# Optimization experiments

Hardware: AMD Instinct MI355X
Metric: run time of the kernel (lower is better)

Reference implementation:

```python
import jax, jax.numpy as jnp
import numpy as np

B, S = 8, 1024          # sequences, uniform seqlen (cu_seqlens = arange(B+1)*S)
H, HID = 16, 2048       # num_heads, hidden_size
D = HID // H            # head_size = 128


def setup_inputs() -> dict:
    key = jax.random.key(0)
    k0, k1, k2 = jax.random.split(key, 3)
    T = B * S
    hidden_states = jax.random.normal(k0, (T, HID), jnp.float32)
    # FastLinear after prepare_weights stores weight transposed: [in, out]
    w_attn = jax.random.normal(k1, (HID, HID + 2 * D), jnp.float32) * 0.02
    b_attn = jnp.zeros((HID + 2 * D,), jnp.float32)
    w_proj = jax.random.normal(k2, (HID, HID), jnp.float32) * 0.02
    b_proj = jnp.zeros((HID,), jnp.float32)
    cu_seqlens = jnp.arange(B + 1, dtype=jnp.int32) * S
    layer_past = jnp.zeros((T, 2, 1, D), jnp.float32)
    return {
        "hidden_states": hidden_states,
        "w_attn": w_attn,
        "b_attn": b_attn,
        "w_proj": w_proj,
        "b_proj": b_proj,
        "cu_seqlens": cu_seqlens,
        "max_s": S,
        "layer_past": layer_past,
    }


def reference(hidden_states, w_attn, b_attn, w_proj, b_proj, cu_seqlens, max_s, layer_past):
    # Prefill branch: causal MQA flash attention; layer_past is written (cache)
    # but the returned output does not depend on it.
    scale = D ** -0.5
    qkv = hidden_states @ w_attn + b_attn                 # [T, HID + 2D]
    q = qkv[:, :HID].reshape(B, S, H, D)                  # [B,S,H,D]
    kv = qkv[:, HID:].reshape(B, S, 2, D)
    k = kv[:, :, 0]                                       # [B,S,D] single KV head
    v = kv[:, :, 1]                                       # [B,S,D]
    scores = jnp.einsum('bqhd,bkd->bhqk', q, k) * scale   # [B,H,S,S]
    causal = jnp.tril(jnp.ones((S, S), dtype=bool))
    scores = jnp.where(causal, scores, jnp.finfo(scores.dtype).min)
    probs = jax.nn.softmax(scores, axis=-1)
    attn = jnp.einsum('bhqk,bkd->bqhd', probs, v)         # [B,S,H,D]
    attn = attn.reshape(B * S, HID)
    return attn @ w_proj + b_proj                         # [T, HID]
```

## Files before the change

### kernel.cpp

```cpp
#include <hip/hip_runtime.h>
#include <hip/hip_bf16.h>

typedef __hip_bfloat16 bf16;
typedef __attribute__((ext_vector_type(8))) __bf16 bf16x8;
typedef __attribute__((ext_vector_type(4))) float f32x4;
typedef __attribute__((ext_vector_type(16))) float f32x16;
typedef __attribute__((ext_vector_type(8))) short s16x8;
typedef __attribute__((ext_vector_type(4))) unsigned u32x4;

#define B_    8
#define S_    1024
#define H_    16
#define D_    128
#define HID_  2048
#define NQKV_ 2304
#define T_    8192

__device__ __forceinline__ void gload_lds16(const void* g, void* l) {
  __builtin_amdgcn_global_load_lds((const __attribute__((address_space(1))) void*)g,
                                   (__attribute__((address_space(3))) void*)l, 16, 0, 0);
}

__device__ __forceinline__ unsigned pack_bf16(float lo, float hi) {
  return ((unsigned)__bfloat16_as_ushort(__float2bfloat16(hi)) << 16) |
         (unsigned)__bfloat16_as_ushort(__float2bfloat16(lo));
}

__global__ void cast_bf16_kernel(const float* __restrict__ src, bf16* __restrict__ dst, int n8) {
  const int i = blockIdx.x * 256 + threadIdx.x;
  if (i >= n8) return;
  const float4 a = ((const float4*)src)[2 * i];
  const float4 b = ((const float4*)src)[2 * i + 1];
  s16x8 o;
  o[0] = (short)__bfloat16_as_ushort(__float2bfloat16(a.x));
  o[1] = (short)__bfloat16_as_ushort(__float2bfloat16(a.y));
  o[2] = (short)__bfloat16_as_ushort(__float2bfloat16(a.z));
  o[3] = (short)__bfloat16_as_ushort(__float2bfloat16(a.w));
  o[4] = (short)__bfloat16_as_ushort(__float2bfloat16(b.x));
  o[5] = (short)__bfloat16_as_ushort(__float2bfloat16(b.y));
  o[6] = (short)__bfloat16_as_ushort(__float2bfloat16(b.z));
  o[7] = (short)__bfloat16_as_ushort(__float2bfloat16(b.w));
  ((s16x8*)dst)[i] = o;
}

__global__ void transpose_cast_kernel(const float* __restrict__ src, bf16* __restrict__ dst,
                                      int R, int C) {
  __shared__ float tile[32][33];
  const int tx = threadIdx.x & 31, ty = threadIdx.x >> 5;
  const int rt = blockIdx.y * 32, ct = blockIdx.x * 32;
#pragma unroll
  for (int k = 0; k < 4; ++k)
    tile[ty + 8 * k][tx] = src[(size_t)(rt + ty + 8 * k) * C + ct + tx];
  __syncthreads();
#pragma unroll
  for (int k = 0; k < 4; ++k)
    dst[(size_t)(ct + ty + 8 * k) * R + rt + tx] = __float2bfloat16(tile[tx][ty + 8 * k]);
}

__global__ void transpose_v_kernel(const bf16* __restrict__ QKV, bf16* __restrict__ Vt) {
  __shared__ short t[64][72];
  const int kt = blockIdx.x, dt = blockIdx.y, b = blockIdx.z;
  const int r = threadIdx.x >> 3;
  const int c8 = (threadIdx.x & 7) * 8;
#pragma unroll
  for (int p = 0; p < 2; ++p) {
    const int row = p * 32 + r;
    const s16x8 v = *(const s16x8*)(QKV + (size_t)(b * S_ + kt * 64 + row) * NQKV_ +
                                    HID_ + D_ + dt * 64 + c8);
    *(s16x8*)&t[row][c8] = v;
  }
  __syncthreads();
#pragma unroll
  for (int p = 0; p < 2; ++p) {
    const int drow = p * 32 + r;
    s16x8 o;
#pragma unroll
    for (int j = 0; j < 8; ++j) o[j] = t[c8 + j][drow];
    *(s16x8*)(Vt + (size_t)(b * D_ + dt * 64 + drow) * S_ + kt * 64 + c8) = o;
  }
}

template <bool OUT_F32>
__global__ __launch_bounds__(256, 2) void gemm_kernel(const bf16* __restrict__ A,
                                                      const bf16* __restrict__ Bt,
                                                      const float* __restrict__ bias,
                                                      void* __restrict__ Cout,
                                                      int M, int N, int K) {
  __shared__ char lds[65536];
  const int tid = threadIdx.x;
  const int lane = tid & 63;
  const int wave = tid >> 6;

  const int gx = gridDim.x;
  const int lid = blockIdx.y * gx + blockIdx.x;
  const int cpx = (gx * gridDim.y) >> 3;
  const int swz = (lid & 7) * cpx + (lid >> 3);
  const int bn = swz % gx, bm = swz / gx;

  const int lrow = lane & 15, lk = lane >> 4;
  const int rbase = (wave >> 1) * 64;
  const int nbase = (wave & 1) * 64;
  f32x4 acc[4][4] = {};

  int srow[4], scol[4];
#pragma unroll
  for (int o = 0; o < 4; ++o) {
    const int X = o * 4096 + tid * 16;
    const int r = X >> 7, Y = X & 127;
    srow[o] = r;
    scol[o] = Y ^ ((r & 7) << 4);
  }

  const char* Ab = (const char*)A + (size_t)(bm * 128) * K * 2;
  const char* Bb = (const char*)Bt + (size_t)(bn * 128) * K * 2;

#define G_STAGE(buf, kt_)                                                              \
  _Pragma("unroll") for (int o = 0; o < 4; ++o)                                        \
      gload_lds16(Ab + (size_t)srow[o] * (K * 2) + (size_t)(kt_) * 128 + scol[o],      \
                  lds + (buf) + o * 4096 + tid * 16);                                  \
  _Pragma("unroll") for (int o = 0; o < 4; ++o)                                        \
      gload_lds16(Bb + (size_t)srow[o] * (K * 2) + (size_t)(kt_) * 128 + scol[o],      \
                  lds + (buf) + 16384 + o * 4096 + tid * 16);

  G_STAGE(0, 0);

  const int nkt = K >> 6;
  for (int kt = 0; kt < nkt; ++kt) {
    const int cur = (kt & 1) * 32768;
    if (kt < nkt - 1) {
      G_STAGE(cur ^ 32768, kt + 1);
      asm volatile("s_waitcnt vmcnt(8)" ::: "memory");
    } else {
      asm volatile("s_waitcnt vmcnt(0)" ::: "memory");
    }
    __builtin_amdgcn_s_barrier();

    bf16x8 af[4][2], bfr[4][2];
#pragma unroll
    for (int mi = 0; mi < 4; ++mi) {
      const int row = rbase + mi * 16 + lrow;
#pragma unroll
      for (int kk = 0; kk < 2; ++kk)
        af[mi][kk] =
            *(const bf16x8*)(lds + cur + row * 128 + ((kk * 64 + lk * 16) ^ ((row & 7) << 4)));
    }
#pragma unroll
    for (int ni = 0; ni < 4; ++ni) {
      const int row = nbase + ni * 16 + lrow;
#pragma unroll
      for (int kk = 0; kk < 2; ++kk)
        bfr[ni][kk] = *(const bf16x8*)(lds + cur + 16384 + row * 128 +
                                       ((kk * 64 + lk * 16) ^ ((row & 7) << 4)));
    }
#pragma unroll
    for (int kk = 0; kk < 2; ++kk)
#pragma unroll
      for (int mi = 0; mi < 4; ++mi)
#pragma unroll
        for (int ni = 0; ni < 4; ++ni)
          acc[mi][ni] =
              __builtin_amdgcn_mfma_f32_16x16x32_bf16(af[mi][kk], bfr[ni][kk], acc[mi][ni], 0, 0, 0);
    __builtin_amdgcn_s_barrier();
  }
#undef G_STAGE

#pragma unroll
  for (int ni = 0; ni < 4; ++ni) {
    const int col = bn * 128 + nbase + ni * 16 + lrow;
    const float bv = bias[col];
#pragma unroll
    for (int mi = 0; mi < 4; ++mi) {
      const int row0 = bm * 128 + rbase + mi * 16 + lk * 4;
#pragma unroll
      for (int r = 0; r < 4; ++r) {
        const float v = acc[mi][ni][r] + bv;
        if (OUT_F32)
          ((float*)Cout)[(size_t)(row0 + r) * N + col] = v;
        else
          ((bf16*)Cout)[(size_t)(row0 + r) * N + col] = __float2bfloat16(v);
      }
    }
  }
}

__global__ __launch_bounds__(512, 2) void attn_kernel(const bf16* __restrict__ QKV,
                                                      const bf16* __restrict__ Vt,
                                                      bf16* __restrict__ aout) {
  const int pairid = blockIdx.x;
  const int h = blockIdx.y;
  const int b = blockIdx.z;
  const int tid = threadIdx.x;
  const int l = tid & 63;
  const int w = tid >> 6;
  const int ql = l & 31;
  const int hi = l >> 5;

  __shared__ char lds[49152];

  const char* qkv_b = (const char*)QKV + (size_t)b * S_ * (NQKV_ * 2);
  const char* vt_b = (const char*)Vt + (size_t)b * D_ * S_ * 2;

  int kr[2], kc[2], vr[2], vc[2];
#pragma unroll
  for (int o = 0; o < 2; ++o) {
    const int X = o * 8192 + tid * 16;
    const int r = X >> 8;
    kr[o] = r;
    kc[o] = (X & 255) ^ ((r & 15) << 4);
    const int d = X >> 7;
    vr[o] = d;
    vc[o] = (X & 127) ^ ((d & 7) << 4);
  }

#define STAGE_K(kb_off, kt_)                                                          \
  _Pragma("unroll") for (int o = 0; o < 2; ++o)                                       \
      gload_lds16(qkv_b + (size_t)((kt_) * 64 + kr[o]) * (NQKV_ * 2) + HID_ * 2 +     \
                      kc[o],                                                          \
                  lds + (kb_off) + o * 8192 + tid * 16);
#define STAGE_V(kt_)                                                                  \
  _Pragma("unroll") for (int o = 0; o < 2; ++o)                                       \
      gload_lds16(vt_b + (size_t)vr[o] * (S_ * 2) + (kt_) * 128 + vc[o],              \
                  lds + 32768 + o * 8192 + tid * 16);

  for (int pass = 0; pass < 2; ++pass) {
    const int qt = pass == 0 ? (3 - pairid) : pairid;

    bf16x8 qf[8];
#pragma unroll
    for (int p = 0; p < 2; ++p) {
#pragma unroll
      for (int o = 0; o < 4; ++o) {
        const int X = o * 8192 + tid * 16;
        const int r = X >> 8;
        const int cb = (X & 255) ^ ((r & 15) << 4);
        gload_lds16(qkv_b + (size_t)(qt * 256 + p * 128 + r) * (NQKV_ * 2) + h * 256 + cb,
                    lds + X);
      }
      asm volatile("s_waitcnt vmcnt(0)" ::: "memory");
      __builtin_amdgcn_s_barrier();
      if ((w >> 2) == p) {
        const int qrow = (w & 3) * 32 + ql;
#pragma unroll
        for (int ds = 0; ds < 8; ++ds)
          qf[ds] = *(const bf16x8*)(lds + qrow * 256 + ((ds * 32 + hi * 16) ^ ((qrow & 15) << 4)));
      }
      asm volatile("s_waitcnt lgkmcnt(0)" ::: "memory");
      __builtin_amdgcn_sched_barrier(0);
      __builtin_amdgcn_s_barrier();
    }

    STAGE_K(0, 0);

    const float scale = 0.08838834764831845f;
    const int qglob = qt * 256 + w * 32 + ql;
    float mrun = -1e30f, lrun = 0.f;
    f32x16 Oacc[4] = {};

    const int nkt = 4 * qt + 4;
    for (int kt = 0; kt < nkt; ++kt) {
      const int kb = (kt & 1) * 16384;
      STAGE_V(kt);
      if (kt < nkt - 1) {
        STAGE_K(kb ^ 16384, kt + 1);
        asm volatile("s_waitcnt vmcnt(4)" ::: "memory");
      } else {
        asm volatile("s_waitcnt vmcnt(2)" ::: "memory");
      }
      __builtin_amdgcn_s_barrier();
      __builtin_amdgcn_sched_barrier(0);

      const bool skip = (64 * kt >= 256 * qt + 32 * w + 32);
      bf16x8 pa[4];
      if (!skip) {
        const bool need_mask = (64 * kt + 63 > 256 * qt + 32 * w);

        f32x16 s0 = {}, s1 = {};
        __builtin_amdgcn_s_setprio(1);
#pragma unroll
        for (int ds = 0; ds < 8; ++ds) {
          const int krow = ql;
          const bf16x8 kf =
              *(const bf16x8*)(lds + kb + krow * 256 + ((ds * 32 + hi * 16) ^ ((krow & 15) << 4)));
          s0 = __builtin_amdgcn_mfma_f32_32x32x16_bf16(kf, qf[ds], s0, 0, 0, 0);
        }
#pragma unroll
        for (int ds = 0; ds < 8; ++ds) {
          const int krow = 32 + ql;
          const bf16x8 kf =
              *(const bf16x8*)(lds + kb + krow * 256 + ((ds * 32 + hi * 16) ^ ((krow & 15) << 4)));
          s1 = __builtin_amdgcn_mfma_f32_32x32x16_bf16(kf, qf[ds], s1, 0, 0, 0);
        }
        __builtin_amdgcn_s_setprio(0);

#pragma unroll
        for (int r = 0; r < 16; ++r) {
          const int krl = (r & 3) + 8 * (r >> 2) + 4 * hi;
          float v0 = s0[r] * scale, v1 = s1[r] * scale;
          if (need_mask) {
            if (64 * kt + krl > qglob) v0 = -1e30f;
            if (64 * kt + 32 + krl > qglob) v1 = -1e30f;
          }
          s0[r] = v0;
          s1[r] = v1;
        }

        float a0 = -1e30f, a1 = -1e30f, a2 = -1e30f, a3 = -1e30f;
#pragma unroll
        for (int r = 0; r < 16; r += 4) {
          a0 = fmaxf(a0, fmaxf(s0[r], s1[r]));
          a1 = fmaxf(a1, fmaxf(s0[r + 1], s1[r + 1]));
          a2 = fmaxf(a2, fmaxf(s0[r + 2], s1[r + 2]));
          a3 = fmaxf(a3, fmaxf(s0[r + 3], s1[r + 3]));
        }
        float tmax = fmaxf(fmaxf(a0, a1), fmaxf(a2, a3));
        tmax = fmaxf(tmax, __shfl_xor(tmax, 32));

        if (!__all(tmax <= mrun + 8.f)) {
          const float mn = fmaxf(mrun, tmax);
          const float corr = __expf(mrun - mn);
          mrun = mn;
          lrun *= corr;
#pragma unroll
          for (int r = 0; r < 16; ++r) {
            const float cq = __shfl(corr, (r & 3) + 8 * (r >> 2) + 4 * hi);
#pragma unroll
            for (int dt = 0; dt < 4; ++dt) Oacc[dt][r] *= cq;
          }
        }

        float b0 = 0.f, b1 = 0.f, b2 = 0.f, b3 = 0.f;
#pragma unroll
        for (int r = 0; r < 16; r += 4) {
          s0[r] = __expf(s0[r] - mrun);
          s1[r] = __expf(s1[r] - mrun);
          b0 += s0[r] + s1[r];
          s0[r + 1] = __expf(s0[r + 1] - mrun);
          s1[r + 1] = __expf(s1[r + 1] - mrun);
          b1 += s0[r + 1] + s1[r + 1];
          s0[r + 2] = __expf(s0[r + 2] - mrun);
          s1[r + 2] = __expf(s1[r + 2] - mrun);
          b2 += s0[r + 2] + s1[r + 2];
          s0[r + 3] = __expf(s0[r + 3] - mrun);
          s1[r + 3] = __expf(s1[r + 3] - mrun);
          b3 += s0[r + 3] + s1[r + 3];
        }
        float rs = (b0 + b1) + (b2 + b3);
        rs += __shfl_xor(rs, 32);
        lrun += rs;

        unsigned c[16], xc[16];
#pragma unroll
        for (int m = 0; m < 8; ++m) {
          c[m] = pack_bf16(s0[2 * m], s0[2 * m + 1]);
          c[8 + m] = pack_bf16(s1[2 * m], s1[2 * m + 1]);
        }
#pragma unroll
        for (int m = 0; m < 16; ++m) xc[m] = (unsigned)__shfl_xor((int)c[m], 32);

#pragma unroll
        for (int kh = 0; kh < 2; ++kh) {
          const int base = 8 * kh;
          u32x4 f0, f1;
          f0[0] = hi ? xc[base + 2] : c[base + 0];
          f0[1] = hi ? xc[base + 3] : c[base + 1];
          f0[2] = hi ? c[base + 2] : xc[base + 0];
          f0[3] = hi ? c[base + 3] : xc[base + 1];
          f1[0] = hi ? xc[base + 6] : c[base + 4];
          f1[1] = hi ? xc[base + 7] : c[base + 5];
          f1[2] = hi ? c[base + 6] : xc[base + 4];
          f1[3] = hi ? c[base + 7] : xc[base + 5];
          pa[2 * kh] = __builtin_bit_cast(bf16x8, f0);
          pa[2 * kh + 1] = __builtin_bit_cast(bf16x8, f1);
        }
      }

      if (kt < nkt - 1)
        asm volatile("s_waitcnt vmcnt(2)" ::: "memory");
      else
        asm volatile("s_waitcnt vmcnt(0)" ::: "memory");
      __builtin_amdgcn_s_barrier();
      __builtin_amdgcn_sched_barrier(0);

      if (!skip) {
        __builtin_amdgcn_s_setprio(1);
#pragma unroll
        for (int dt = 0; dt < 4; ++dt) {
          const int vrow = dt * 32 + ql;
#pragma unroll
          for (int ks = 0; ks < 4; ++ks) {
            const bf16x8 vf = *(const bf16x8*)(lds + 32768 + vrow * 128 +
                                               ((ks * 32 + hi * 16) ^ ((vrow & 7) << 4)));
            Oacc[dt] = __builtin_amdgcn_mfma_f32_32x32x16_bf16(pa[ks], vf, Oacc[dt], 0, 0, 0);
          }
        }
        __builtin_amdgcn_s_setprio(0);
      }
      __builtin_amdgcn_s_barrier();
    }

#pragma unroll
    for (int r = 0; r < 16; ++r) {
      const int qi = (r & 3) + 8 * (r >> 2) + 4 * hi;
      const float lr = __shfl(lrun, qi);
      const float inv = 1.0f / lr;
      const int token = b * S_ + qt * 256 + w * 32 + qi;
      bf16* orow = aout + (size_t)token * HID_ + h * D_;
#pragma unroll
      for (int dt = 0; dt < 4; ++dt)
        orow[dt * 32 + ql] = __float2bfloat16(Oacc[dt][r] * inv);
    }
    __builtin_amdgcn_s_barrier();
  }
#undef STAGE_K
#undef STAGE_V
}

extern "C" void kernel_launch(void* const* d_in, const int* in_sizes, int n_in,
                              void* d_out, int out_size, void* d_ws, size_t ws_size,
                              hipStream_t stream) {
  const float* hidden = (const float*)d_in[0];
  const float* w_attn = (const float*)d_in[1];
  const float* b_attn = (const float*)d_in[2];
  const float* w_proj = (const float*)d_in[3];
  const float* b_proj = (const float*)d_in[4];

  char* ws = (char*)d_ws;
  char* dob = (char*)d_out;

  bf16* Xbf = (bf16*)ws;
  bf16* WpT = (bf16*)(ws + 33554432);
  bf16* QKV = (bf16*)dob;
  bf16* WaT = (bf16*)(dob + 37748736);
  bf16* Vt = (bf16*)(dob + 50331648);

  cast_bf16_kernel<<<(T_ * HID_) / 8 / 256, 256, 0, stream>>>(hidden, Xbf, (T_ * HID_) / 8);
  transpose_cast_kernel<<<dim3(NQKV_ / 32, HID_ / 32), 256, 0, stream>>>(w_attn, WaT, HID_, NQKV_);
  transpose_cast_kernel<<<dim3(HID_ / 32, HID_ / 32), 256, 0, stream>>>(w_proj, WpT, HID_, HID_);

  gemm_kernel<false><<<dim3(NQKV_ / 128, T_ / 128), 256, 0, stream>>>(
      Xbf, WaT, b_attn, QKV, T_, NQKV_, HID_);

  transpose_v_kernel<<<dim3(S_ / 64, D_ / 64, B_), 256, 0, stream>>>(QKV, Vt);

  attn_kernel<<<dim3(2, H_, B_), 512, 0, stream>>>(QKV, Vt, Xbf);

  gemm_kernel<true><<<dim3(HID_ / 128, T_ / 128), 256, 0, stream>>>(
      Xbf, WpT, b_proj, (float*)d_out, T_, HID_, HID_);
}
```

Measured before the change: 263.1 us.

## Enlarge GEMM tiles to 256x256 with 8 waves and phased load/MFMA interleave

The bf16 GEMM kernel moves from 128x128 tiles with 4 waves to 256x256 tiles with 8 waves and 128KB of double-buffered LDS. Each K-step is split into four sub-tile MFMA phases, with prefetch of the next stage issued in halves between them and MFMA priority raised via setprio. The aim is more data reuse per byte loaded and better overlap of global loads with MFMA work. The cost is fewer workgroups (for example 9x32 for the QKV GEMM), likely occupancy of one block per CU given the LDS size, and more barriers per K-step.

```diff
diff --git a/kernel.cpp b/kernel.cpp
--- a/kernel.cpp
+++ b/kernel.cpp
@@ -81,15 +81,18 @@
 }
 
 template <bool OUT_F32>
-__global__ __launch_bounds__(256, 2) void gemm_kernel(const bf16* __restrict__ A,
+__global__ __launch_bounds__(512, 2) void gemm_kernel(const bf16* __restrict__ A,
                                                       const bf16* __restrict__ Bt,
                                                       const float* __restrict__ bias,
                                                       void* __restrict__ Cout,
                                                       int M, int N, int K) {
-  __shared__ char lds[65536];
+  __shared__ char lds[131072];
   const int tid = threadIdx.x;
   const int lane = tid & 63;
   const int wave = tid >> 6;
+  const int wm = wave >> 2;
+  const int wn = wave & 3;
+  const int lrow = lane & 15, lk = lane >> 4;
 
   const int gx = gridDim.x;
   const int lid = blockIdx.y * gx + blockIdx.x;
@@ -97,90 +100,114 @@
   const int swz = (lid & 7) * cpx + (lid >> 3);
   const int bn = swz % gx, bm = swz / gx;
 
-  const int lrow = lane & 15, lk = lane >> 4;
-  const int rbase = (wave >> 1) * 64;
-  const int nbase = (wave & 1) * 64;
-  f32x4 acc[4][4] = {};
-
-  int srow[4], scol[4];
-#pragma unroll
-  for (int o = 0; o < 4; ++o) {
-    const int X = o * 4096 + tid * 16;
-    const int r = X >> 7, Y = X & 127;
+  f32x4 acc[2][2][4][2] = {};
+
+  int srow[2], scol[2];
+#pragma unroll
+  for (int o = 0; o < 2; ++o) {
+    const int X = o * 8192 + tid * 16;
+    const int r = X >> 7;
     srow[o] = r;
-    scol[o] = Y ^ ((r & 7) << 4);
-  }
-
-  const char* Ab = (const char*)A + (size_t)(bm * 128) * K * 2;
-  const char* Bb = (const char*)Bt + (size_t)(bn * 128) * K * 2;
-
-#define G_STAGE(buf, kt_)                                                              \
-  _Pragma("unroll") for (int o = 0; o < 4; ++o)                                        \
-      gload_lds16(Ab + (size_t)srow[o] * (K * 2) + (size_t)(kt_) * 128 + scol[o],      \
-                  lds + (buf) + o * 4096 + tid * 16);                                  \
-  _Pragma("unroll") for (int o = 0; o < 4; ++o)                                        \
-      gload_lds16(Bb + (size_t)srow[o] * (K * 2) + (size_t)(kt_) * 128 + scol[o],      \
-                  lds + (buf) + 16384 + o * 4096 + tid * 16);
-
-  G_STAGE(0, 0);
-
+    scol[o] = (X & 127) ^ ((r & 7) << 4);
+  }
+
+  const char* Ab = (const char*)A + (size_t)(bm * 256) * K * 2;
+  const char* Bb = (const char*)Bt + (size_t)(bn * 256) * K * 2;
+
+#define STG_HALF(src_base, matoff, half, cbuf, kt_)                                     \
+  _Pragma("unroll") for (int o = 0; o < 2; ++o)                                         \
+      gload_lds16((src_base) + (size_t)((half) * 128 + srow[o]) * (K * 2) +             \
+                      (size_t)(kt_) * 128 + scol[o],                                    \
+                  lds + (cbuf) + (matoff) + (half) * 16384 + o * 8192 + tid * 16);
+
+#define RD_A(cbuf, msub)                                                                \
+  _Pragma("unroll") for (int mi = 0; mi < 4; ++mi)                                      \
+  _Pragma("unroll") for (int kk = 0; kk < 2; ++kk) {                                    \
+    const int row = (msub) * 128 + wm * 64 + mi * 16 + lrow;                            \
+    af[msub][mi][kk] = *(const bf16x8*)(lds + (cbuf) + row * 128 +                      \
+                                        ((kk * 64 + lk * 16) ^ ((row & 7) << 4)));      \
+  }
+#define RD_B(cbuf, nsub)                                                                \
+  _Pragma("unroll") for (int ni = 0; ni < 2; ++ni)                                      \
+  _Pragma("unroll") for (int kk = 0; kk < 2; ++kk) {                                    \
+    const int row = (nsub) * 128 + wn * 32 + ni * 16 + lrow;                            \
+    bf[nsub][ni][kk] = *(const bf16x8*)(lds + (cbuf) + 32768 + row * 128 +              \
+                                        ((kk * 64 + lk * 16) ^ ((row & 7) << 4)));      \
+  }
+#define PH_MFMA(MS, NS)                                                                 \
+  asm volatile("s_waitcnt lgkmcnt(0)" ::: "memory");                                    \
+  __builtin_amdgcn_sched_barrier(0);                                                    \
+  __builtin_amdgcn_s_setprio(1);                                                        \
+  _Pragma("unroll") for (int kk = 0; kk < 2; ++kk)                                      \
+  _Pragma("unroll") for (int mi = 0; mi < 4; ++mi)                                      \
+  _Pragma("unroll") for (int ni = 0; ni < 2; ++ni)                                      \
+    acc[MS][NS][mi][ni] = __builtin_amdgcn_mfma_f32_16x16x32_bf16(                      \
+        af[MS][mi][kk], bf[NS][ni][kk], acc[MS][NS][mi][ni], 0, 0, 0);                  \
+  __builtin_amdgcn_s_setprio(0);
+
+  STG_HALF(Ab, 0, 0, 0, 0);
+  STG_HALF(Ab, 0, 1, 0, 0);
+  STG_HALF(Bb, 32768, 0, 0, 0);
+  STG_HALF(Bb, 32768, 1, 0, 0);
+
+  bf16x8 af[2][4][2], bf[2][2][2];
   const int nkt = K >> 6;
   for (int kt = 0; kt < nkt; ++kt) {
-    const int cur = (kt & 1) * 32768;
-    if (kt < nkt - 1) {
-      G_STAGE(cur ^ 32768, kt + 1);
-      asm volatile("s_waitcnt vmcnt(8)" ::: "memory");
-    } else {
+    const int cb = (kt & 1) * 65536;
+    const int nb = cb ^ 65536;
+    const bool pre = (kt + 1 < nkt);
+    asm volatile("s_waitcnt vmcnt(2)" ::: "memory");
+    __builtin_amdgcn_s_barrier();
+    RD_A(cb, 0);
+    RD_B(cb, 0);
+    if (pre) STG_HALF(Ab, 0, 0, nb, kt + 1);
+    __builtin_amdgcn_s_barrier();
+    PH_MFMA(0, 0);
+    __builtin_amdgcn_s_barrier();
+    RD_A(cb, 1);
+    if (pre) STG_HALF(Ab, 0, 1, nb, kt + 1);
+    __builtin_amdgcn_s_barrier();
+    PH_MFMA(1, 0);
+    if (pre)
+      asm volatile("s_waitcnt vmcnt(4)" ::: "memory");
+    else
       asm volatile("s_waitcnt vmcnt(0)" ::: "memory");
-    }
-    __builtin_amdgcn_s_barrier();
-
-    bf16x8 af[4][2], bfr[4][2];
-#pragma unroll
-    for (int mi = 0; mi < 4; ++mi) {
-      const int row = rbase + mi * 16 + lrow;
-#pragma unroll
-      for (int kk = 0; kk < 2; ++kk)
-        af[mi][kk] =
-            *(const bf16x8*)(lds + cur + row * 128 + ((kk * 64 + lk * 16) ^ ((row & 7) << 4)));
-    }
-#pragma unroll
-    for (int ni = 0; ni < 4; ++ni) {
-      const int row = nbase + ni * 16 + lrow;
-#pragma unroll
-      for (int kk = 0; kk < 2; ++kk)
-        bfr[ni][kk] = *(const bf16x8*)(lds + cur + 16384 + row * 128 +
-                                       ((kk * 64 + lk * 16) ^ ((row & 7) << 4)));
-    }
-#pragma unroll
-    for (int kk = 0; kk < 2; ++kk)
-#pragma unroll
-      for (int mi = 0; mi < 4; ++mi)
-#pragma unroll
-        for (int ni = 0; ni < 4; ++ni)
-          acc[mi][ni] =
-              __builtin_amdgcn_mfma_f32_16x16x32_bf16(af[mi][kk], bfr[ni][kk], acc[mi][ni], 0, 0, 0);
-    __builtin_amdgcn_s_barrier();
-  }
-#undef G_STAGE
-
-#pragma unroll
-  for (int ni = 0; ni < 4; ++ni) {
-    const int col = bn * 128 + nbase + ni * 16 + lrow;
-    const float bv = bias[col];
-#pragma unroll
-    for (int mi = 0; mi < 4; ++mi) {
-      const int row0 = bm * 128 + rbase + mi * 16 + lk * 4;
-#pragma unroll
-      for (int r = 0; r < 4; ++r) {
-        const float v = acc[mi][ni][r] + bv;
-        if (OUT_F32)
-          ((float*)Cout)[(size_t)(row0 + r) * N + col] = v;
-        else
-          ((bf16*)Cout)[(size_t)(row0 + r) * N + col] = __float2bfloat16(v);
-      }
-    }
-  }
+    __builtin_amdgcn_s_barrier();
+    RD_B(cb, 1);
+    if (pre) STG_HALF(Bb, 32768, 0, nb, kt + 1);
+    __builtin_amdgcn_s_barrier();
+    PH_MFMA(0, 1);
+    __builtin_amdgcn_s_barrier();
+    if (pre) STG_HALF(Bb, 32768, 1, nb, kt + 1);
+    PH_MFMA(1, 1);
+    __builtin_amdgcn_s_barrier();
+  }
+#undef STG_HALF
+#undef RD_A
+#undef RD_B
+#undef PH_MFMA
+
+#pragma unroll
+  for (int ms = 0; ms < 2; ++ms)
+#pragma unroll
+    for (int ns = 0; ns < 2; ++ns)
+#pragma unroll
+      for (int ni = 0; ni < 2; ++ni) {
+        const int col = bn * 256 + ns * 128 + wn * 32 + ni * 16 + lrow;
+        const float bv = bias[col];
+#pragma unroll
+        for (int mi = 0; mi < 4; ++mi) {
+          const int row0 = bm * 256 + ms * 128 + wm * 64 + mi * 16 + lk * 4;
+#pragma unroll
+          for (int r = 0; r < 4; ++r) {
+            const float v = acc[ms][ns][mi][ni][r] + bv;
+            if (OUT_F32)
+              ((float*)Cout)[(size_t)(row0 + r) * N + col] = v;
+            else
+              ((bf16*)Cout)[(size_t)(row0 + r) * N + col] = __float2bfloat16(v);
+          }
+        }
+      }
 }
 
 __global__ __launch_bounds__(512, 2) void attn_kernel(const bf16* __restrict__ QKV,
@@ -437,13 +464,13 @@
   transpose_cast_kernel<<<dim3(NQKV_ / 32, HID_ / 32), 256, 0, stream>>>(w_attn, WaT, HID_, NQKV_);
   transpose_cast_kernel<<<dim3(HID_ / 32, HID_ / 32), 256, 0, stream>>>(w_proj, WpT, HID_, HID_);
 
-  gemm_kernel<false><<<dim3(NQKV_ / 128, T_ / 128), 256, 0, stream>>>(
+  gemm_kernel<false><<<dim3(NQKV_ / 256, T_ / 256), 512, 0, stream>>>(
       Xbf, WaT, b_attn, QKV, T_, NQKV_, HID_);
 
   transpose_v_kernel<<<dim3(S_ / 64, D_ / 64, B_), 256, 0, stream>>>(QKV, Vt);
 
   attn_kernel<<<dim3(2, H_, B_), 512, 0, stream>>>(QKV, Vt, Xbf);
 
-  gemm_kernel<true><<<dim3(HID_ / 128, T_ / 128), 256, 0, stream>>>(
+  gemm_kernel<true><<<dim3(HID_ / 256, T_ / 256), 512, 0, stream>>>(
       Xbf, WpT, b_proj, (float*)d_out, T_, HID_, HID_);
 }
```

After: 274.7 us. 4.4% more time.
